# Kernel tuning notes

Hardware: AMD Instinct MI355X
Metric: run time of the kernel (lower is better)

The kernel has to match this reference:

```python
import jax, jax.numpy as jnp
import numpy as np
import math

B, S, D_IN, EMBED, H = 4, 1024, 1024, 1024, 16
HD = EMBED // H  # 64


def setup_inputs() -> dict:
    key = jax.random.key(0)
    ks = jax.random.split(key, 8)
    x = jax.random.normal(ks[0], (B, S, D_IN), dtype=jnp.float32)
    mask = jax.random.randint(ks[1], (B, S, S), 0, 2, dtype=jnp.int32)
    weights = jax.random.uniform(ks[2], (B, S, S), dtype=jnp.float32)
    # xavier-uniform-ish scale for projections
    lim_qkv = math.sqrt(6.0 / (D_IN + 3 * EMBED))
    lim_o = math.sqrt(6.0 / (EMBED + EMBED))
    W_qkv = jax.random.uniform(ks[3], (3 * EMBED, D_IN), minval=-lim_qkv, maxval=lim_qkv, dtype=jnp.float32)
    b_qkv = jnp.zeros((3 * EMBED,), dtype=jnp.float32)
    W_o = jax.random.uniform(ks[4], (EMBED, EMBED), minval=-lim_o, maxval=lim_o, dtype=jnp.float32)
    b_o = jnp.zeros((EMBED,), dtype=jnp.float32)
    return {"x": x, "mask": mask, "weights": weights, "W_qkv": W_qkv, "b_qkv": b_qkv, "W_o": W_o, "b_o": b_o}


def reference(x, mask, weights, W_qkv, b_qkv, W_o, b_o):
    b, s, _ = x.shape
    # QKV projection: [b, s, 3*EMBED] -> [b, H, s, 3*HD]
    qkv = (x @ W_qkv.T + b_qkv).reshape(b, s, H, 3 * HD).transpose(0, 2, 1, 3)
    q, k, v = jnp.split(qkv, 3, axis=-1)  # each [b, H, s, HD]
    logits = jnp.einsum('bhqd,bhkd->bhqk', q, k) / math.sqrt(HD)
    logits = jnp.where(mask[:, None, :, :] == 0, jnp.float32(-9e15), logits)
    # weights transposed on last two dims, broadcast over heads
    w = jnp.swapaxes(weights, -2, -1)[:, None, :, :]  # [b, 1, s, s]
    m = jnp.max(logits, axis=-1, keepdims=True)
    e = w * jnp.exp(logits - m)
    attn = e / jnp.sum(e, axis=-1, keepdims=True)
    vals = jnp.einsum('bhqk,bhkd->bhqd', attn, v)
    vals = vals.transpose(0, 2, 1, 3).reshape(b, s, EMBED)
    return vals @ W_o.T + b_o
```

## Files before the change

### kernel.cpp

```cpp
#include <hip/hip_runtime.h>
#include <hip/hip_bf16.h>
#include <stdint.h>

#define SDIM 1024
#define BATCH 4
#define NH 16
#define HDIM 64
#define KDIM 1024
#define N_QKV 3072
#define EMB 1024

typedef uint16_t u16;
typedef __attribute__((ext_vector_type(4))) float f32x4;
typedef __attribute__((ext_vector_type(8))) short bf16x8;
typedef __attribute__((ext_vector_type(8))) unsigned short u16x8;

__device__ __forceinline__ u16 f2bf(float f) {
  union { float f; uint32_t u; } x; x.f = f;
  uint32_t r = x.u + 0x7FFFu + ((x.u >> 16) & 1u);
  return (u16)(r >> 16);
}

__device__ __forceinline__ float bf2f(u16 b) {
  union { uint32_t u; float f; } x; x.u = ((uint32_t)b) << 16;
  return x.f;
}

__device__ __forceinline__ void gload_lds16(const u16* g, u16* l) {
  __builtin_amdgcn_global_load_lds(
      (const __attribute__((address_space(1))) unsigned int*)g,
      (__attribute__((address_space(3))) unsigned int*)l, 16, 0, 0);
}

#define N8_X  524288
#define N8_WQ 393216
#define N8_WO 131072
__global__ void cvt3_kernel(const float* __restrict__ a, const float* __restrict__ b,
                            const float* __restrict__ c,
                            u16* __restrict__ oa, u16* __restrict__ ob, u16* __restrict__ oc) {
  const int total = N8_X + N8_WQ + N8_WO;
  int stride = gridDim.x * blockDim.x;
  for (int i = blockIdx.x * blockDim.x + threadIdx.x; i < total; i += stride) {
    const float* s; u16* d; int j;
    if (i < N8_X)            { s = a; d = oa; j = i; }
    else if (i < N8_X + N8_WQ){ s = b; d = ob; j = i - N8_X; }
    else                     { s = c; d = oc; j = i - N8_X - N8_WQ; }
    const float4* s4 = (const float4*)s + (size_t)j * 2;
    float4 u = s4[0], v = s4[1];
    u16x8 o;
    o[0] = f2bf(u.x); o[1] = f2bf(u.y); o[2] = f2bf(u.z); o[3] = f2bf(u.w);
    o[4] = f2bf(v.x); o[5] = f2bf(v.y); o[6] = f2bf(v.z); o[7] = f2bf(v.w);
    ((u16x8*)d)[j] = o;
  }
}

__global__ __launch_bounds__(512, 1) void gemm_qkv_wm3(
    const u16* __restrict__ A, const u16* __restrict__ Bm,
    const float* __restrict__ bias,
    u16* __restrict__ Qh, u16* __restrict__ Kh, u16* __restrict__ Vt,
    const int* __restrict__ mask, const float* __restrict__ wts, u16* __restrict__ wm3)
{
  __shared__ char smem[131072];
  const int tid = threadIdx.x;
  const int gid = blockIdx.x;
  const int brow = (gid & 15) * 256, bcol = (gid >> 4) * 192;
  const int wid = tid >> 6, lane = tid & 63;
  const int g = lane >> 4, c = lane & 15, cx = c & 7;
  const int wr = wid & 3, wc = wid >> 2;

  const u16* asrc[4]; int adoff[4];
  #pragma unroll
  for (int j = 0; j < 4; ++j) {
    int i = j * 512 + tid;
    int row = i >> 3, sch = (i & 7) ^ (row & 7);
    asrc[j] = A + (size_t)(brow + row) * KDIM + sch * 8;
    adoff[j] = (j * 512 + wid * 64) * 16;
  }
  const u16* bsrc[3]; int bdoff[3];
  #pragma unroll
  for (int j = 0; j < 3; ++j) {
    int i = j * 512 + tid;
    int row = i >> 3, sch = (i & 7) ^ (row & 7);
    bsrc[j] = Bm + (size_t)(bcol + row) * KDIM + sch * 8;
    bdoff[j] = 32768 + (j * 512 + wid * 64) * 16;
  }

  auto stage = [&](int kt, int slot) {
    char* base = smem + slot * 57344;
    #pragma unroll
    for (int j = 0; j < 4; ++j)
      gload_lds16(asrc[j] + kt * 64, (u16*)(base + adoff[j]));
    #pragma unroll
    for (int j = 0; j < 3; ++j)
      gload_lds16(bsrc[j] + kt * 64, (u16*)(base + bdoff[j]));
  };

  stage(0, 0);

  {
    const size_t SS = (size_t)SDIM * SDIM;
    int   (*mt)[69] = (int(*)[69])(smem + 57344);
    float (*wt)[69] = (float(*)[69])(smem + 57344 + 17664);

    #pragma unroll
    for (int tt = 0; tt < 4; ++tt) {
      const int id = gid * 4 + tt;
      const int kt = id & 15, qt = (id >> 4) & 15, b = id >> 8;
      const int q0 = qt * 64, k0 = kt * 64;
      if (tt) __syncthreads();

      #pragma unroll
      for (int j = 0; j < 2; ++j) {
        int idx = j * 512 + tid;
        int row = idx >> 4, c4 = idx & 15;
        int4 m4 = *(const int4*)(mask + (size_t)b * SS + (size_t)(q0 + row) * SDIM + k0 + c4 * 4);
        mt[row][c4 * 4 + 0] = m4.x; mt[row][c4 * 4 + 1] = m4.y;
        mt[row][c4 * 4 + 2] = m4.z; mt[row][c4 * 4 + 3] = m4.w;
        float4 w4 = *(const float4*)(wts + (size_t)b * SS + (size_t)(k0 + row) * SDIM + q0 + c4 * 4);
        wt[row][c4 * 4 + 0] = w4.x; wt[row][c4 * 4 + 1] = w4.y;
        wt[row][c4 * 4 + 2] = w4.z; wt[row][c4 * 4 + 3] = w4.w;
      }
      __syncthreads();

      const int wid2 = tid >> 7, hf = (tid >> 6) & 1, lane2 = tid & 63;
      const int g2 = lane2 >> 4, c2 = lane2 & 15;
      const int ql = wid2 * 16 + c2;
      u16x8 o;
      #pragma unroll
      for (int e = 0; e < 8; ++e) {
        int kl = 8 * g2 + 4 * (e >> 2) + (e & 3) + 32 * hf;
        o[e] = mt[ql][kl] ? f2bf(wt[kl][ql]) : (u16)0;
      }
      size_t off = ((((size_t)(b * 16 + qt) * 4 + wid2) * 16 + kt)) * 1024 + lane2 * 16 + hf * 8;
      *(u16x8*)(wm3 + off) = o;
    }
    __syncthreads();
  }

  f32x4 acc[4][6] = {};

  for (int kt = 0; kt < 16; ++kt) {
    if (kt < 15) stage(kt + 1, (kt + 1) & 1);

    const char* As = smem + (kt & 1) * 57344;
    const char* Bs = As + 32768;

    #pragma unroll
    for (int kk = 0; kk < 2; ++kk) {
      bf16x8 af[4], bfr[6];
      #pragma unroll
      for (int m = 0; m < 4; ++m) {
        int row = wr * 64 + m * 16 + c;
        af[m] = *(const bf16x8*)(As + (row << 7) + ((((kk << 2) + g) ^ cx) << 4));
      }
      #pragma unroll
      for (int n = 0; n < 6; ++n) {
        int row = wc * 96 + n * 16 + c;
        bfr[n] = *(const bf16x8*)(Bs + (row << 7) + ((((kk << 2) + g) ^ cx) << 4));
      }
      __builtin_amdgcn_s_setprio(1);
      #pragma unroll
      for (int m = 0; m < 4; ++m)
        #pragma unroll
        for (int n = 0; n < 6; ++n)
          acc[m][n] = __builtin_amdgcn_mfma_f32_16x16x32_bf16(
              af[m], bfr[n], acc[m][n], 0, 0, 0);
      __builtin_amdgcn_s_setprio(0);
    }
    __syncthreads();
  }

  #pragma unroll
  for (int m = 0; m < 4; ++m) {
    #pragma unroll
    for (int n = 0; n < 6; ++n) {
      int col = bcol + wc * 96 + n * 16 + c;
      float bv = bias[col];
      int h = col / 192;
      int rem = col - h * 192;
      int sec = rem >> 6, d = rem & 63;
      #pragma unroll
      for (int r = 0; r < 4; ++r) {
        int row = brow + wr * 64 + m * 16 + g * 4 + r;
        int b = row >> 10, sl = row & 1023;
        float v = acc[m][n][r] + bv;
        if (sec == 0)
          Qh[((size_t)(b * NH + h) * SDIM + sl) * HDIM + d] = f2bf(v * 0.125f);
        else if (sec == 1)
          Kh[((size_t)(b * NH + h) * SDIM + sl) * HDIM + d] = f2bf(v);
        else
          Vt[((size_t)(b * NH + h) * HDIM + d) * SDIM + sl] = f2bf(v);
      }
    }
  }
}

__global__ __launch_bounds__(256) void gemm_bt(
    const u16* __restrict__ A, const u16* __restrict__ Bm,
    const float* __restrict__ bias, float* __restrict__ C,
    int M, int N, int K)
{
  __shared__ u16 As[128 * 64];
  __shared__ u16 Bs[128 * 64];
  const int tid = threadIdx.x;
  const int wid = tid >> 6, lane = tid & 63;
  const int g = lane >> 4, c = lane & 15, cx = c & 7;
  const int wrow = (wid >> 1) * 64, wcol = (wid & 1) * 64;
  const int brow = blockIdx.x * 128, bcol = blockIdx.y * 128;

  const u16* asrc[4]; const u16* bsrc[4]; u16* adst[4]; u16* bdst[4];
  #pragma unroll
  for (int j = 0; j < 4; ++j) {
    int ci = j * 256 + tid;
    int row = ci >> 3, sch = (ci & 7) ^ (row & 7);
    asrc[j] = A  + (size_t)(brow + row) * K + sch * 8;
    bsrc[j] = Bm + (size_t)(bcol + row) * K + sch * 8;
    adst[j] = As + (j * 256 + wid * 64) * 8;
    bdst[j] = Bs + (j * 256 + wid * 64) * 8;
  }

  f32x4 acc[4][4] = {};
  const char* Asc = (const char*)As;
  const char* Bsc = (const char*)Bs;

  for (int kt = 0; kt < K / 64; ++kt) {
    #pragma unroll
    for (int j = 0; j < 4; ++j) {
      gload_lds16(asrc[j] + kt * 64, adst[j]);
      gload_lds16(bsrc[j] + kt * 64, bdst[j]);
    }
    __syncthreads();

    bf16x8 af[2][4], bfr[2][4];
    #pragma unroll
    for (int kk = 0; kk < 2; ++kk)
      #pragma unroll
      for (int i = 0; i < 4; ++i) {
        int cha = ((kk << 2) + g) ^ cx;
        af[kk][i]  = *(const bf16x8*)(Asc + ((wrow + i * 16 + c) << 7) + (cha << 4));
        bfr[kk][i] = *(const bf16x8*)(Bsc + ((wcol + i * 16 + c) << 7) + (cha << 4));
      }
    #pragma unroll
    for (int kk = 0; kk < 2; ++kk)
      #pragma unroll
      for (int mi = 0; mi < 4; ++mi)
        #pragma unroll
        for (int ni = 0; ni < 4; ++ni)
          acc[mi][ni] = __builtin_amdgcn_mfma_f32_16x16x32_bf16(
              af[kk][mi], bfr[kk][ni], acc[mi][ni], 0, 0, 0);
    __syncthreads();
  }

  #pragma unroll
  for (int mi = 0; mi < 4; ++mi)
    #pragma unroll
    for (int ni = 0; ni < 4; ++ni) {
      int col = bcol + wcol + ni * 16 + c;
      float bv = bias[col];
      #pragma unroll
      for (int r = 0; r < 4; ++r) {
        int row = brow + wrow + mi * 16 + g * 4 + r;
        C[(size_t)row * N + col] = acc[mi][ni][r] + bv;
      }
    }
}

__global__ __launch_bounds__(256, 4) void attn_kernel(
    const u16* __restrict__ Qh, const u16* __restrict__ Kh, const u16* __restrict__ Vt,
    const u16* __restrict__ wm3, u16* __restrict__ vals)
{
  int bid = blockIdx.x;
  int swz = (bid & 7) * 128 + (bid >> 3);
  const int qt = swz & 15, bh = swz >> 4;
  const int h = bh & 15, b = bh >> 4;

  const int tid = threadIdx.x;
  const int wid = tid >> 6, lane = tid & 63;
  const int g = lane >> 4, c = lane & 15;
  const int qloc = qt * 64 + wid * 16;

  __shared__ u16 Kb[2][4096];
  __shared__ u16 Vb[2][4096];

  const u16* qp = Qh + ((size_t)bh * SDIM + qloc + c) * HDIM;
  bf16x8 qa0 = *(const bf16x8*)(qp + g * 8);
  bf16x8 qa1 = *(const bf16x8*)(qp + 32 + g * 8);

  const u16* kbase = Kh + (size_t)bh * SDIM * HDIM;
  const u16* vbase = Vt + (size_t)bh * HDIM * SDIM;
  const u16* wbase = wm3 + (((size_t)(b * 16 + qt) * 4 + wid) * 16) * 1024 + lane * 16;

  float l_run = 0.f;
  f32x4 acc_o[4] = {};

  auto fsw = [](int row) { return ((row ^ (row >> 3)) & 7) ^ ((row & 1) << 2); };

  int kro[4], kxr[4], vro[4], vxr[4];
  #pragma unroll
  for (int st = 0; st < 4; ++st) {
    int kr = ((c >> 2) << 3) + ((st & 1) << 2) + (c & 3) + ((st >> 1) << 5);
    kro[st] = kr << 7;
    kxr[st] = fsw(kr);
  }
  #pragma unroll
  for (int dt = 0; dt < 4; ++dt) {
    int vr = dt * 16 + c;
    vro[dt] = vr << 7;
    vxr[dt] = fsw(vr);
  }

  auto stage = [&](int buf, int kt) {
    const int k0 = kt * 64;
    #pragma unroll
    for (int j = 0; j < 2; ++j) {
      int i = j * 256 + tid;
      int row = i >> 3;
      int sch = (i & 7) ^ (((row ^ (row >> 3)) & 7) ^ ((row & 1) << 2));
      gload_lds16(kbase + (size_t)(k0 + row) * HDIM + sch * 8,
                  &Kb[buf][(size_t)(j * 256 + wid * 64) * 8]);
      gload_lds16(vbase + (size_t)row * SDIM + k0 + sch * 8,
                  &Vb[buf][(size_t)(j * 256 + wid * 64) * 8]);
    }
  };

  stage(0, 0);
  __syncthreads();
  int cur = 0;

  for (int kt = 0; kt < 16; ++kt) {
    if (kt < 15) stage(cur ^ 1, kt + 1);

    u16x8 w0 = *(const u16x8*)(wbase + kt * 1024);
    u16x8 w1 = *(const u16x8*)(wbase + kt * 1024 + 8);

    const char* kb = (const char*)&Kb[cur][0];
    const char* vb = (const char*)&Vb[cur][0];

    f32x4 sc[4];
    #pragma unroll
    for (int st = 0; st < 4; ++st) {
      bf16x8 ka0 = *(const bf16x8*)(kb + kro[st] + ((g ^ kxr[st]) << 4));
      bf16x8 ka1 = *(const bf16x8*)(kb + kro[st] + (((4 + g) ^ kxr[st]) << 4));
      f32x4 z = {};
      z = __builtin_amdgcn_mfma_f32_16x16x32_bf16(ka0, qa0, z, 0, 0, 0);
      z = __builtin_amdgcn_mfma_f32_16x16x32_bf16(ka1, qa1, z, 0, 0, 0);
      sc[st] = z;
    }

    float p[4][4];
    #pragma unroll
    for (int st = 0; st < 4; ++st) {
      #pragma unroll
      for (int r = 0; r < 4; ++r) {
        u16 wv = (st < 2) ? ((const u16*)&w0)[st * 4 + r]
                          : ((const u16*)&w1)[(st - 2) * 4 + r];
        float pv = bf2f(wv) * __expf(sc[st][r]);
        p[st][r] = pv;
        l_run += pv;
      }
    }

    uint32_t pk[8];
    #pragma unroll
    for (int i = 0; i < 8; ++i) {
      float lo = p[i >> 1][(i & 1) * 2], hi = p[i >> 1][(i & 1) * 2 + 1];
      asm("v_cvt_pk_bf16_f32 %0, %1, %2" : "=v"(pk[i]) : "v"(lo), "v"(hi));
    }
    union PA { uint32_t u[4]; bf16x8 v; } a0, a1;
    #pragma unroll
    for (int i = 0; i < 4; ++i) { a0.u[i] = pk[i]; a1.u[i] = pk[4 + i]; }

    #pragma unroll
    for (int dt = 0; dt < 4; ++dt) {
      bf16x8 vb0 = *(const bf16x8*)(vb + vro[dt] + ((g ^ vxr[dt]) << 4));
      bf16x8 vb1 = *(const bf16x8*)(vb + vro[dt] + (((4 + g) ^ vxr[dt]) << 4));
      acc_o[dt] = __builtin_amdgcn_mfma_f32_16x16x32_bf16(a0.v, vb0, acc_o[dt], 0, 0, 0);
      acc_o[dt] = __builtin_amdgcn_mfma_f32_16x16x32_bf16(a1.v, vb1, acc_o[dt], 0, 0, 0);
    }

    __syncthreads();
    cur ^= 1;
  }

  l_run += __shfl_xor(l_run, 16);
  l_run += __shfl_xor(l_run, 32);

  float inv[4];
  #pragma unroll
  for (int r = 0; r < 4; ++r)
    inv[r] = 1.0f / __shfl(l_run, g * 4 + r);

  #pragma unroll
  for (int dt = 0; dt < 4; ++dt)
    #pragma unroll
    for (int r = 0; r < 4; ++r) {
      int row = b * SDIM + qloc + g * 4 + r;
      vals[(size_t)row * EMB + h * HDIM + dt * 16 + c] = f2bf(acc_o[dt][r] * inv[r]);
    }
}

extern "C" void kernel_launch(void* const* d_in, const int* in_sizes, int n_in,
                              void* d_out, int out_size, void* d_ws, size_t ws_size,
                              hipStream_t stream) {
  const float* x     = (const float*)d_in[0];
  const int*   mask  = (const int*)d_in[1];
  const float* wts   = (const float*)d_in[2];
  const float* W_qkv = (const float*)d_in[3];
  const float* b_qkv = (const float*)d_in[4];
  const float* W_o   = (const float*)d_in[5];
  const float* b_o   = (const float*)d_in[6];
  float* out = (float*)d_out;

  char* ws = (char*)d_ws;
  u16* xb   = (u16*)(ws);
  u16* wqb  = (u16*)(ws + (8ull  << 20));
  u16* wob  = (u16*)(ws + (14ull << 20));
  u16* Qh   = (u16*)(ws + (16ull << 20));
  u16* Kh   = (u16*)(ws + (24ull << 20));
  u16* Vt   = (u16*)(ws + (32ull << 20));
  u16* valb = (u16*)(ws + (40ull << 20));
  u16* wm3b = (u16*)d_out;

  cvt3_kernel<<<2048, 256, 0, stream>>>(x, W_qkv, W_o, xb, wqb, wob);

  gemm_qkv_wm3<<<256, 512, 0, stream>>>(xb, wqb, b_qkv, Qh, Kh, Vt, mask, wts, wm3b);

  attn_kernel<<<1024, 256, 0, stream>>>(Qh, Kh, Vt, wm3b, valb);

  dim3 g3(32, 8);
  gemm_bt<<<g3, 256, 0, stream>>>(valb, wob, b_o, out, BATCH * SDIM, EMB, KDIM);
}
```

Baseline: 106.8 us.

## Move mask/weight prep into convert kernel and double query rows per attention wave

```diff
diff --git a/kernel.cpp b/kernel.cpp
--- a/kernel.cpp
+++ b/kernel.cpp
@@ -35,32 +35,58 @@
 #define N8_X  524288
 #define N8_WQ 393216
 #define N8_WO 131072
-__global__ void cvt3_kernel(const float* __restrict__ a, const float* __restrict__ b,
-                            const float* __restrict__ c,
-                            u16* __restrict__ oa, u16* __restrict__ ob, u16* __restrict__ oc) {
-  const int total = N8_X + N8_WQ + N8_WO;
+#define NCVT  1048576
+#define NWM3  262144
+__global__ void prep_kernel(const float* __restrict__ a, const float* __restrict__ bq,
+                            const float* __restrict__ co,
+                            u16* __restrict__ oa, u16* __restrict__ ob, u16* __restrict__ oc,
+                            const int* __restrict__ mask, const float* __restrict__ wts,
+                            u16* __restrict__ wm3) {
+  const int total = NCVT + NWM3;
+  const size_t SS = (size_t)SDIM * SDIM;
   int stride = gridDim.x * blockDim.x;
   for (int i = blockIdx.x * blockDim.x + threadIdx.x; i < total; i += stride) {
-    const float* s; u16* d; int j;
-    if (i < N8_X)            { s = a; d = oa; j = i; }
-    else if (i < N8_X + N8_WQ){ s = b; d = ob; j = i - N8_X; }
-    else                     { s = c; d = oc; j = i - N8_X - N8_WQ; }
-    const float4* s4 = (const float4*)s + (size_t)j * 2;
-    float4 u = s4[0], v = s4[1];
-    u16x8 o;
-    o[0] = f2bf(u.x); o[1] = f2bf(u.y); o[2] = f2bf(u.z); o[3] = f2bf(u.w);
-    o[4] = f2bf(v.x); o[5] = f2bf(v.y); o[6] = f2bf(v.z); o[7] = f2bf(v.w);
-    ((u16x8*)d)[j] = o;
-  }
-}
-
-__global__ __launch_bounds__(512, 1) void gemm_qkv_wm3(
+    if (i < NCVT) {
+      const float* s; u16* d; int j;
+      if (i < N8_X)             { s = a;  d = oa; j = i; }
+      else if (i < N8_X + N8_WQ){ s = bq; d = ob; j = i - N8_X; }
+      else                      { s = co; d = oc; j = i - N8_X - N8_WQ; }
+      const float4* s4 = (const float4*)s + (size_t)j * 2;
+      float4 u = s4[0], v = s4[1];
+      u16x8 o;
+      o[0] = f2bf(u.x); o[1] = f2bf(u.y); o[2] = f2bf(u.z); o[3] = f2bf(u.w);
+      o[4] = f2bf(v.x); o[5] = f2bf(v.y); o[6] = f2bf(v.z); o[7] = f2bf(v.w);
+      ((u16x8*)d)[j] = o;
+    } else {
+      int t = i - NCVT;
+      int lane = t & 63, kt = (t >> 6) & 15, T = (t >> 10) & 63, b = t >> 16;
+      int g2 = lane >> 4, c2 = lane & 15;
+      int q = T * 16 + c2;
+      const int* mrow = mask + (size_t)b * SS + (size_t)q * SDIM;
+      const float* wcol = wts + (size_t)b * SS + q;
+      u16* dst = wm3 + ((size_t)(b * 64 + T) * 16 + kt) * 1024 + lane * 16;
+      #pragma unroll
+      for (int hf = 0; hf < 2; ++hf) {
+        int bk = kt * 64 + 8 * g2 + 32 * hf;
+        int4 m0 = *(const int4*)(mrow + bk);
+        int4 m1 = *(const int4*)(mrow + bk + 4);
+        int mm[8] = {m0.x, m0.y, m0.z, m0.w, m1.x, m1.y, m1.z, m1.w};
+        u16x8 o;
+        #pragma unroll
+        for (int e = 0; e < 8; ++e)
+          o[e] = mm[e] ? f2bf(wcol[(size_t)(bk + e) * SDIM]) : (u16)0;
+        *(u16x8*)(dst + hf * 8) = o;
+      }
+    }
+  }
+}
+
+__global__ __launch_bounds__(512, 1) void gemm_qkv(
     const u16* __restrict__ A, const u16* __restrict__ Bm,
     const float* __restrict__ bias,
-    u16* __restrict__ Qh, u16* __restrict__ Kh, u16* __restrict__ Vt,
-    const int* __restrict__ mask, const float* __restrict__ wts, u16* __restrict__ wm3)
+    u16* __restrict__ Qh, u16* __restrict__ Kh, u16* __restrict__ Vt)
 {
-  __shared__ char smem[131072];
+  __shared__ char smem[114688];
   const int tid = threadIdx.x;
   const int gid = blockIdx.x;
   const int brow = (gid & 15) * 256, bcol = (gid >> 4) * 192;
@@ -95,49 +121,10 @@
       gload_lds16(bsrc[j] + kt * 64, (u16*)(base + bdoff[j]));
   };
 
+  f32x4 acc[4][6] = {};
+
   stage(0, 0);
-
-  {
-    const size_t SS = (size_t)SDIM * SDIM;
-    int   (*mt)[69] = (int(*)[69])(smem + 57344);
-    float (*wt)[69] = (float(*)[69])(smem + 57344 + 17664);
-
-    #pragma unroll
-    for (int tt = 0; tt < 4; ++tt) {
-      const int id = gid * 4 + tt;
-      const int kt = id & 15, qt = (id >> 4) & 15, b = id >> 8;
-      const int q0 = qt * 64, k0 = kt * 64;
-      if (tt) __syncthreads();
-
-      #pragma unroll
-      for (int j = 0; j < 2; ++j) {
-        int idx = j * 512 + tid;
-        int row = idx >> 4, c4 = idx & 15;
-        int4 m4 = *(const int4*)(mask + (size_t)b * SS + (size_t)(q0 + row) * SDIM + k0 + c4 * 4);
-        mt[row][c4 * 4 + 0] = m4.x; mt[row][c4 * 4 + 1] = m4.y;
-        mt[row][c4 * 4 + 2] = m4.z; mt[row][c4 * 4 + 3] = m4.w;
-        float4 w4 = *(const float4*)(wts + (size_t)b * SS + (size_t)(k0 + row) * SDIM + q0 + c4 * 4);
-        wt[row][c4 * 4 + 0] = w4.x; wt[row][c4 * 4 + 1] = w4.y;
-        wt[row][c4 * 4 + 2] = w4.z; wt[row][c4 * 4 + 3] = w4.w;
-      }
-      __syncthreads();
-
-      const int wid2 = tid >> 7, hf = (tid >> 6) & 1, lane2 = tid & 63;
-      const int g2 = lane2 >> 4, c2 = lane2 & 15;
-      const int ql = wid2 * 16 + c2;
-      u16x8 o;
-      #pragma unroll
-      for (int e = 0; e < 8; ++e) {
-        int kl = 8 * g2 + 4 * (e >> 2) + (e & 3) + 32 * hf;
-        o[e] = mt[ql][kl] ? f2bf(wt[kl][ql]) : (u16)0;
-      }
-      size_t off = ((((size_t)(b * 16 + qt) * 4 + wid2) * 16 + kt)) * 1024 + lane2 * 16 + hf * 8;
-      *(u16x8*)(wm3 + off) = o;
-    }
-    __syncthreads();
-  }
-
-  f32x4 acc[4][6] = {};
+  __syncthreads();
 
   for (int kt = 0; kt < 16; ++kt) {
     if (kt < 15) stage(kt + 1, (kt + 1) & 1);
@@ -265,33 +252,42 @@
     }
 }
 
-__global__ __launch_bounds__(256, 4) void attn_kernel(
+__global__ __launch_bounds__(256, 2) void attn_kernel(
     const u16* __restrict__ Qh, const u16* __restrict__ Kh, const u16* __restrict__ Vt,
     const u16* __restrict__ wm3, u16* __restrict__ vals)
 {
   int bid = blockIdx.x;
-  int swz = (bid & 7) * 128 + (bid >> 3);
-  const int qt = swz & 15, bh = swz >> 4;
+  int swz = (bid & 7) * 64 + (bid >> 3);
+  const int qt8 = swz & 7, bh = swz >> 3;
   const int h = bh & 15, b = bh >> 4;
 
   const int tid = threadIdx.x;
   const int wid = tid >> 6, lane = tid & 63;
   const int g = lane >> 4, c = lane & 15;
-  const int qloc = qt * 64 + wid * 16;
+  const int qbase = qt8 * 128 + wid * 32;
 
   __shared__ u16 Kb[2][4096];
   __shared__ u16 Vb[2][4096];
 
-  const u16* qp = Qh + ((size_t)bh * SDIM + qloc + c) * HDIM;
-  bf16x8 qa0 = *(const bf16x8*)(qp + g * 8);
-  bf16x8 qa1 = *(const bf16x8*)(qp + 32 + g * 8);
+  bf16x8 qa[2][2];
+  #pragma unroll
+  for (int sub = 0; sub < 2; ++sub) {
+    const u16* qp = Qh + ((size_t)bh * SDIM + qbase + sub * 16 + c) * HDIM;
+    qa[sub][0] = *(const bf16x8*)(qp + g * 8);
+    qa[sub][1] = *(const bf16x8*)(qp + 32 + g * 8);
+  }
 
   const u16* kbase = Kh + (size_t)bh * SDIM * HDIM;
   const u16* vbase = Vt + (size_t)bh * HDIM * SDIM;
-  const u16* wbase = wm3 + (((size_t)(b * 16 + qt) * 4 + wid) * 16) * 1024 + lane * 16;
-
-  float l_run = 0.f;
-  f32x4 acc_o[4] = {};
+  const u16* wbase[2];
+  #pragma unroll
+  for (int sub = 0; sub < 2; ++sub) {
+    int T = qt8 * 8 + wid * 2 + sub;
+    wbase[sub] = wm3 + ((size_t)(b * 64 + T) * 16) * 1024 + lane * 16;
+  }
+
+  float l_run[2] = {0.f, 0.f};
+  f32x4 acc[2][4] = {};
 
   auto fsw = [](int row) { return ((row ^ (row >> 3)) & 7) ^ ((row & 1) << 2); };
 
@@ -330,73 +326,77 @@
   for (int kt = 0; kt < 16; ++kt) {
     if (kt < 15) stage(cur ^ 1, kt + 1);
 
-    u16x8 w0 = *(const u16x8*)(wbase + kt * 1024);
-    u16x8 w1 = *(const u16x8*)(wbase + kt * 1024 + 8);
+    u16x8 w0[2], w1[2];
+    #pragma unroll
+    for (int sub = 0; sub < 2; ++sub) {
+      w0[sub] = *(const u16x8*)(wbase[sub] + kt * 1024);
+      w1[sub] = *(const u16x8*)(wbase[sub] + kt * 1024 + 8);
+    }
 
     const char* kb = (const char*)&Kb[cur][0];
     const char* vb = (const char*)&Vb[cur][0];
 
-    f32x4 sc[4];
+    uint32_t pk[2][8];
     #pragma unroll
     for (int st = 0; st < 4; ++st) {
       bf16x8 ka0 = *(const bf16x8*)(kb + kro[st] + ((g ^ kxr[st]) << 4));
       bf16x8 ka1 = *(const bf16x8*)(kb + kro[st] + (((4 + g) ^ kxr[st]) << 4));
-      f32x4 z = {};
-      z = __builtin_amdgcn_mfma_f32_16x16x32_bf16(ka0, qa0, z, 0, 0, 0);
-      z = __builtin_amdgcn_mfma_f32_16x16x32_bf16(ka1, qa1, z, 0, 0, 0);
-      sc[st] = z;
-    }
-
-    float p[4][4];
-    #pragma unroll
-    for (int st = 0; st < 4; ++st) {
-      #pragma unroll
-      for (int r = 0; r < 4; ++r) {
-        u16 wv = (st < 2) ? ((const u16*)&w0)[st * 4 + r]
-                          : ((const u16*)&w1)[(st - 2) * 4 + r];
-        float pv = bf2f(wv) * __expf(sc[st][r]);
-        p[st][r] = pv;
-        l_run += pv;
-      }
-    }
-
-    uint32_t pk[8];
-    #pragma unroll
-    for (int i = 0; i < 8; ++i) {
-      float lo = p[i >> 1][(i & 1) * 2], hi = p[i >> 1][(i & 1) * 2 + 1];
-      asm("v_cvt_pk_bf16_f32 %0, %1, %2" : "=v"(pk[i]) : "v"(lo), "v"(hi));
-    }
-    union PA { uint32_t u[4]; bf16x8 v; } a0, a1;
-    #pragma unroll
-    for (int i = 0; i < 4; ++i) { a0.u[i] = pk[i]; a1.u[i] = pk[4 + i]; }
+      #pragma unroll
+      for (int sub = 0; sub < 2; ++sub) {
+        f32x4 z = {};
+        z = __builtin_amdgcn_mfma_f32_16x16x32_bf16(ka0, qa[sub][0], z, 0, 0, 0);
+        z = __builtin_amdgcn_mfma_f32_16x16x32_bf16(ka1, qa[sub][1], z, 0, 0, 0);
+        float pv[4];
+        #pragma unroll
+        for (int r = 0; r < 4; ++r) {
+          u16 wv = (st < 2) ? ((const u16*)&w0[sub])[st * 4 + r]
+                            : ((const u16*)&w1[sub])[(st - 2) * 4 + r];
+          pv[r] = bf2f(wv) * __expf(z[r]);
+          l_run[sub] += pv[r];
+        }
+        asm("v_cvt_pk_bf16_f32 %0, %1, %2" : "=v"(pk[sub][st * 2])     : "v"(pv[0]), "v"(pv[1]));
+        asm("v_cvt_pk_bf16_f32 %0, %1, %2" : "=v"(pk[sub][st * 2 + 1]) : "v"(pv[2]), "v"(pv[3]));
+      }
+    }
+
+    union PA { uint32_t u[4]; bf16x8 v; } a0[2], a1[2];
+    #pragma unroll
+    for (int sub = 0; sub < 2; ++sub)
+      #pragma unroll
+      for (int i = 0; i < 4; ++i) { a0[sub].u[i] = pk[sub][i]; a1[sub].u[i] = pk[sub][4 + i]; }
 
     #pragma unroll
     for (int dt = 0; dt < 4; ++dt) {
       bf16x8 vb0 = *(const bf16x8*)(vb + vro[dt] + ((g ^ vxr[dt]) << 4));
       bf16x8 vb1 = *(const bf16x8*)(vb + vro[dt] + (((4 + g) ^ vxr[dt]) << 4));
-      acc_o[dt] = __builtin_amdgcn_mfma_f32_16x16x32_bf16(a0.v, vb0, acc_o[dt], 0, 0, 0);
-      acc_o[dt] = __builtin_amdgcn_mfma_f32_16x16x32_bf16(a1.v, vb1, acc_o[dt], 0, 0, 0);
+      #pragma unroll
+      for (int sub = 0; sub < 2; ++sub) {
+        acc[sub][dt] = __builtin_amdgcn_mfma_f32_16x16x32_bf16(a0[sub].v, vb0, acc[sub][dt], 0, 0, 0);
+        acc[sub][dt] = __builtin_amdgcn_mfma_f32_16x16x32_bf16(a1[sub].v, vb1, acc[sub][dt], 0, 0, 0);
+      }
     }
 
     __syncthreads();
     cur ^= 1;
   }
 
-  l_run += __shfl_xor(l_run, 16);
-  l_run += __shfl_xor(l_run, 32);
-
-  float inv[4];
-  #pragma unroll
-  for (int r = 0; r < 4; ++r)
-    inv[r] = 1.0f / __shfl(l_run, g * 4 + r);
-
-  #pragma unroll
-  for (int dt = 0; dt < 4; ++dt)
-    #pragma unroll
-    for (int r = 0; r < 4; ++r) {
-      int row = b * SDIM + qloc + g * 4 + r;
-      vals[(size_t)row * EMB + h * HDIM + dt * 16 + c] = f2bf(acc_o[dt][r] * inv[r]);
-    }
+  #pragma unroll
+  for (int sub = 0; sub < 2; ++sub) {
+    float lr = l_run[sub];
+    lr += __shfl_xor(lr, 16);
+    lr += __shfl_xor(lr, 32);
+    float inv[4];
+    #pragma unroll
+    for (int r = 0; r < 4; ++r)
+      inv[r] = 1.0f / __shfl(lr, g * 4 + r);
+    #pragma unroll
+    for (int dt = 0; dt < 4; ++dt)
+      #pragma unroll
+      for (int r = 0; r < 4; ++r) {
+        int row = b * SDIM + qbase + sub * 16 + g * 4 + r;
+        vals[(size_t)row * EMB + h * HDIM + dt * 16 + c] = f2bf(acc[sub][dt][r] * inv[r]);
+      }
+  }
 }
 
 extern "C" void kernel_launch(void* const* d_in, const int* in_sizes, int n_in,
@@ -421,11 +421,11 @@
   u16* valb = (u16*)(ws + (40ull << 20));
   u16* wm3b = (u16*)d_out;
 
-  cvt3_kernel<<<2048, 256, 0, stream>>>(x, W_qkv, W_o, xb, wqb, wob);
-
-  gemm_qkv_wm3<<<256, 512, 0, stream>>>(xb, wqb, b_qkv, Qh, Kh, Vt, mask, wts, wm3b);
-
-  attn_kernel<<<1024, 256, 0, stream>>>(Qh, Kh, Vt, wm3b, valb);
+  prep_kernel<<<2048, 256, 0, stream>>>(x, W_qkv, W_o, xb, wqb, wob, mask, wts, wm3b);
+
+  gemm_qkv<<<256, 512, 0, stream>>>(xb, wqb, b_qkv, Qh, Kh, Vt);
+
+  attn_kernel<<<512, 256, 0, stream>>>(Qh, Kh, Vt, wm3b, valb);
 
   dim3 g3(32, 8);
   gemm_bt<<<g3, 256, 0, stream>>>(valb, wob, b_o, out, BATCH * SDIM, EMB, KDIM);
```

After: 111.4 us. 1.04x slower.

## Move mask/weights preprocessing from QKV GEMM prologue into conversion kernel

Applied to the files above, without the earlier changes.

```diff
diff --git a/kernel.cpp b/kernel.cpp
--- a/kernel.cpp
+++ b/kernel.cpp
@@ -35,32 +35,58 @@
 #define N8_X  524288
 #define N8_WQ 393216
 #define N8_WO 131072
-__global__ void cvt3_kernel(const float* __restrict__ a, const float* __restrict__ b,
-                            const float* __restrict__ c,
-                            u16* __restrict__ oa, u16* __restrict__ ob, u16* __restrict__ oc) {
-  const int total = N8_X + N8_WQ + N8_WO;
+#define NCVT  1048576
+#define NWM3  262144
+__global__ void prep_kernel(const float* __restrict__ a, const float* __restrict__ bq,
+                            const float* __restrict__ co,
+                            u16* __restrict__ oa, u16* __restrict__ ob, u16* __restrict__ oc,
+                            const int* __restrict__ mask, const float* __restrict__ wts,
+                            u16* __restrict__ wm3) {
+  const int total = NCVT + NWM3;
+  const size_t SS = (size_t)SDIM * SDIM;
   int stride = gridDim.x * blockDim.x;
   for (int i = blockIdx.x * blockDim.x + threadIdx.x; i < total; i += stride) {
-    const float* s; u16* d; int j;
-    if (i < N8_X)            { s = a; d = oa; j = i; }
-    else if (i < N8_X + N8_WQ){ s = b; d = ob; j = i - N8_X; }
-    else                     { s = c; d = oc; j = i - N8_X - N8_WQ; }
-    const float4* s4 = (const float4*)s + (size_t)j * 2;
-    float4 u = s4[0], v = s4[1];
-    u16x8 o;
-    o[0] = f2bf(u.x); o[1] = f2bf(u.y); o[2] = f2bf(u.z); o[3] = f2bf(u.w);
-    o[4] = f2bf(v.x); o[5] = f2bf(v.y); o[6] = f2bf(v.z); o[7] = f2bf(v.w);
-    ((u16x8*)d)[j] = o;
-  }
-}
-
-__global__ __launch_bounds__(512, 1) void gemm_qkv_wm3(
+    if (i < NCVT) {
+      const float* s; u16* d; int j;
+      if (i < N8_X)             { s = a;  d = oa; j = i; }
+      else if (i < N8_X + N8_WQ){ s = bq; d = ob; j = i - N8_X; }
+      else                      { s = co; d = oc; j = i - N8_X - N8_WQ; }
+      const float4* s4 = (const float4*)s + (size_t)j * 2;
+      float4 u = s4[0], v = s4[1];
+      u16x8 o;
+      o[0] = f2bf(u.x); o[1] = f2bf(u.y); o[2] = f2bf(u.z); o[3] = f2bf(u.w);
+      o[4] = f2bf(v.x); o[5] = f2bf(v.y); o[6] = f2bf(v.z); o[7] = f2bf(v.w);
+      ((u16x8*)d)[j] = o;
+    } else {
+      int t = i - NCVT;
+      int lane = t & 63, kt = (t >> 6) & 15, T = (t >> 10) & 63, b = t >> 16;
+      int g2 = lane >> 4, c2 = lane & 15;
+      int q = T * 16 + c2;
+      const int* mrow = mask + (size_t)b * SS + (size_t)q * SDIM;
+      const float* wcol = wts + (size_t)b * SS + q;
+      u16* dst = wm3 + ((size_t)(b * 64 + T) * 16 + kt) * 1024 + lane * 16;
+      #pragma unroll
+      for (int hf = 0; hf < 2; ++hf) {
+        int bk = kt * 64 + 8 * g2 + 32 * hf;
+        int4 m0 = *(const int4*)(mrow + bk);
+        int4 m1 = *(const int4*)(mrow + bk + 4);
+        int mm[8] = {m0.x, m0.y, m0.z, m0.w, m1.x, m1.y, m1.z, m1.w};
+        u16x8 o;
+        #pragma unroll
+        for (int e = 0; e < 8; ++e)
+          o[e] = mm[e] ? f2bf(wcol[(size_t)(bk + e) * SDIM]) : (u16)0;
+        *(u16x8*)(dst + hf * 8) = o;
+      }
+    }
+  }
+}
+
+__global__ __launch_bounds__(512, 1) void gemm_qkv(
     const u16* __restrict__ A, const u16* __restrict__ Bm,
     const float* __restrict__ bias,
-    u16* __restrict__ Qh, u16* __restrict__ Kh, u16* __restrict__ Vt,
-    const int* __restrict__ mask, const float* __restrict__ wts, u16* __restrict__ wm3)
+    u16* __restrict__ Qh, u16* __restrict__ Kh, u16* __restrict__ Vt)
 {
-  __shared__ char smem[131072];
+  __shared__ char smem[114688];
   const int tid = threadIdx.x;
   const int gid = blockIdx.x;
   const int brow = (gid & 15) * 256, bcol = (gid >> 4) * 192;
@@ -95,49 +121,10 @@
       gload_lds16(bsrc[j] + kt * 64, (u16*)(base + bdoff[j]));
   };
 
+  f32x4 acc[4][6] = {};
+
   stage(0, 0);
-
-  {
-    const size_t SS = (size_t)SDIM * SDIM;
-    int   (*mt)[69] = (int(*)[69])(smem + 57344);
-    float (*wt)[69] = (float(*)[69])(smem + 57344 + 17664);
-
-    #pragma unroll
-    for (int tt = 0; tt < 4; ++tt) {
-      const int id = gid * 4 + tt;
-      const int kt = id & 15, qt = (id >> 4) & 15, b = id >> 8;
-      const int q0 = qt * 64, k0 = kt * 64;
-      if (tt) __syncthreads();
-
-      #pragma unroll
-      for (int j = 0; j < 2; ++j) {
-        int idx = j * 512 + tid;
-        int row = idx >> 4, c4 = idx & 15;
-        int4 m4 = *(const int4*)(mask + (size_t)b * SS + (size_t)(q0 + row) * SDIM + k0 + c4 * 4);
-        mt[row][c4 * 4 + 0] = m4.x; mt[row][c4 * 4 + 1] = m4.y;
-        mt[row][c4 * 4 + 2] = m4.z; mt[row][c4 * 4 + 3] = m4.w;
-        float4 w4 = *(const float4*)(wts + (size_t)b * SS + (size_t)(k0 + row) * SDIM + q0 + c4 * 4);
-        wt[row][c4 * 4 + 0] = w4.x; wt[row][c4 * 4 + 1] = w4.y;
-        wt[row][c4 * 4 + 2] = w4.z; wt[row][c4 * 4 + 3] = w4.w;
-      }
-      __syncthreads();
-
-      const int wid2 = tid >> 7, hf = (tid >> 6) & 1, lane2 = tid & 63;
-      const int g2 = lane2 >> 4, c2 = lane2 & 15;
-      const int ql = wid2 * 16 + c2;
-      u16x8 o;
-      #pragma unroll
-      for (int e = 0; e < 8; ++e) {
-        int kl = 8 * g2 + 4 * (e >> 2) + (e & 3) + 32 * hf;
-        o[e] = mt[ql][kl] ? f2bf(wt[kl][ql]) : (u16)0;
-      }
-      size_t off = ((((size_t)(b * 16 + qt) * 4 + wid2) * 16 + kt)) * 1024 + lane2 * 16 + hf * 8;
-      *(u16x8*)(wm3 + off) = o;
-    }
-    __syncthreads();
-  }
-
-  f32x4 acc[4][6] = {};
+  __syncthreads();
 
   for (int kt = 0; kt < 16; ++kt) {
     if (kt < 15) stage(kt + 1, (kt + 1) & 1);
@@ -421,9 +408,9 @@
   u16* valb = (u16*)(ws + (40ull << 20));
   u16* wm3b = (u16*)d_out;
 
-  cvt3_kernel<<<2048, 256, 0, stream>>>(x, W_qkv, W_o, xb, wqb, wob);
-
-  gemm_qkv_wm3<<<256, 512, 0, stream>>>(xb, wqb, b_qkv, Qh, Kh, Vt, mask, wts, wm3b);
+  prep_kernel<<<2048, 256, 0, stream>>>(x, W_qkv, W_o, xb, wqb, wob, mask, wts, wm3b);
+
+  gemm_qkv<<<256, 512, 0, stream>>>(xb, wqb, b_qkv, Qh, Kh, Vt);
 
   attn_kernel<<<1024, 256, 0, stream>>>(Qh, Kh, Vt, wm3b, valb);
 
```

Measured after the change: 108.9 us. Within noise of the previous version (+2.0%).
